# Optimization experiments

Measured on AMD Instinct MI355X. Metric: run time of the kernel, lower is better.

Reference implementation:

```python
import jax, jax.numpy as jnp
import numpy as np

HQ, HKV, D, RD = 32, 8, 128, 64   # q heads, kv heads, head_dim, rotary_dim
EPS = 1e-6


def _rms_norm(x, w, eps):
    # per-head RMSNorm over last dim (non-gemma: scale by w)
    var = jnp.mean(x * x, axis=-1, keepdims=True)
    return x * jax.lax.rsqrt(var + eps) * w


def _partial_rope(x, c, s, rd):
    # x: [T, H, D]; c/s: [T, rd//2]; NeoX half-split rotation on first rd dims
    x1 = x[..., : rd // 2]
    x2 = x[..., rd // 2 : rd]
    c = c[:, None, :]
    s = s[:, None, :]
    return jnp.concatenate([x1 * c - x2 * s, x2 * c + x1 * s, x[..., rd:]], axis=-1)


def setup_inputs() -> dict:
    key = jax.random.key(0)
    ks = jax.random.split(key, 6)
    B, QL, HID, CACHE = 4, 512, 4096, 512
    T = B * QL
    MAXPOS = 4096
    NPAGES, PS, MP = 256, 16, 64  # total pages, page_size, max pages per seq

    hidden_states = jax.random.normal(ks[0], (T, HID), jnp.float32)
    inv = 1.0 / (10000.0 ** (np.arange(0, RD, 2, dtype=np.float64) / RD))
    ang = np.arange(MAXPOS)[:, None] * inv[None, :]
    cos = jnp.asarray(np.cos(ang), jnp.float32)   # [MAXPOS, RD//2]
    sin = jnp.asarray(np.sin(ang), jnp.float32)
    positions = jnp.tile(CACHE + jnp.arange(QL, dtype=jnp.int32), B)  # [T]
    k_cache = jax.random.normal(ks[1], (NPAGES, PS, HKV, D), jnp.float32)
    v_cache = jax.random.normal(ks[2], (NPAGES, PS, HKV, D), jnp.float32)
    page_table = jnp.arange(B * MP, dtype=jnp.int32).reshape(B, MP)
    cache_seqlens = jnp.full((B,), CACHE, jnp.int32)
    cu_seqlens_q = jnp.arange(B + 1, dtype=jnp.int32) * QL
    qkv_weight = jax.random.normal(ks[3], ((HQ + 2 * HKV) * D, HID), jnp.float32) * 0.02
    o_proj_weight = jax.random.normal(ks[4], (HID, HQ * D), jnp.float32) * 0.02
    q_norm_weight = jnp.ones((D,), jnp.float32)
    k_norm_weight = jnp.ones((D,), jnp.float32)
    return dict(hidden_states=hidden_states, cos=cos, sin=sin, positions=positions,
                k_cache=k_cache, v_cache=v_cache, page_table=page_table,
                cache_seqlens=cache_seqlens, cu_seqlens_q=cu_seqlens_q,
                qkv_weight=qkv_weight, o_proj_weight=o_proj_weight,
                q_norm_weight=q_norm_weight, k_norm_weight=k_norm_weight)


def reference(hidden_states, cos, sin, positions, k_cache, v_cache, page_table,
              cache_seqlens, cu_seqlens_q, qkv_weight, o_proj_weight,
              q_norm_weight, k_norm_weight):
    T = hidden_states.shape[0]
    B = cache_seqlens.shape[0]
    QL = T // B                       # equal-length sequences (extend mode)
    PS = k_cache.shape[1]

    # QKV projection + split
    qkv = hidden_states @ qkv_weight.T
    q, k, v = jnp.split(qkv, [HQ * D, (HQ + HKV) * D], axis=-1)

    # per-head QK RMSNorm (q_norm_weight.shape[0] == head_dim branch)
    q = _rms_norm(q.reshape(T, HQ, D), q_norm_weight, EPS)
    k = _rms_norm(k.reshape(T, HKV, D), k_norm_weight, EPS)
    v = v.reshape(T, HKV, D)

    # partial RoPE
    pc, psn = cos[positions], sin[positions]
    q = _partial_rope(q, pc, psn, RD)
    k = _partial_rope(k, pc, psn, RD)

    # paged KV-cache write: absolute slot = cache_seqlens[b] + j
    pos_abs = cache_seqlens[:, None] + jnp.arange(QL, dtype=jnp.int32)[None, :]  # [B,QL]
    pages = jnp.take_along_axis(page_table, pos_abs // PS, axis=1)
    slots = pos_abs % PS
    k_cache = k_cache.at[pages, slots].set(k.reshape(B, QL, HKV, D))
    v_cache = v_cache.at[pages, slots].set(v.reshape(B, QL, HKV, D))

    # gather per-sequence KV from pages: [B, KV, HKV, D]
    KV = page_table.shape[1] * PS
    keys = k_cache[page_table].reshape(B, KV, HKV, D)
    vals = v_cache[page_table].reshape(B, KV, HKV, D)

    # GQA paged attention with causal mask on absolute positions
    G = HQ // HKV
    qh = q.reshape(B, QL, HKV, G, D)
    scale = 1.0 / np.sqrt(D).astype(np.float32)
    scores = jnp.einsum('bqhgd,bkhd->bhgqk', qh, keys) * scale
    kpos = jnp.arange(KV, dtype=jnp.int32)
    mask = kpos[None, None, :] <= pos_abs[:, :, None]                  # [B,QL,KV]
    scores = jnp.where(mask[:, None, None, :, :], scores, -1e30)
    probs = jax.nn.softmax(scores, axis=-1)
    attn = jnp.einsum('bhgqk,bkhd->bqhgd', probs, vals).reshape(T, HQ * D)

    return attn @ o_proj_weight.T
```

## Files before the change

### kernel.cpp

```cpp
#include <hip/hip_runtime.h>

typedef unsigned int   u32;
typedef unsigned short u16;

typedef float  f32x4  __attribute__((ext_vector_type(4)));
typedef u32    u32x4  __attribute__((ext_vector_type(4)));
typedef u16    u16x4  __attribute__((ext_vector_type(4)));
typedef __bf16 bf16x8 __attribute__((ext_vector_type(8)));

union FragU { u16 us[8]; u32x4 q; bf16x8 v; };

__device__ __forceinline__ u32 f2u(float x){ union{float f;u32 u;}c; c.f=x; return c.u; }
__device__ __forceinline__ float u2f(u32 u){ union{float f;u32 u;}c; c.u=u; return c.f; }
__device__ __forceinline__ u16 bfhi(float x){ u32 u=f2u(x); return (u16)((u + 0x7fffu + ((u>>16)&1u))>>16); }
__device__ __forceinline__ float bff(u16 h){ return u2f(((u32)h)<<16); }

__device__ __forceinline__ void gload16(const void* g, void* l){
  __builtin_amdgcn_global_load_lds(
      (const __attribute__((address_space(1))) unsigned int*)g,
      (__attribute__((address_space(3))) unsigned int*)l, 16, 0, 0);
}

__global__ __launch_bounds__(256)
void bf16_pack3(const float* __restrict__ s0, u16* __restrict__ d0, int n0,
                const float* __restrict__ s1, u16* __restrict__ d1, int n1,
                const float* __restrict__ s2, u16* __restrict__ d2, int n2)
{
  const int total = n0 + n1 + n2;
  for (int i = blockIdx.x*256 + threadIdx.x; i < total; i += gridDim.x*256){
    const float* s; u16* d; int j = i;
    if (j < n0)            { s = s0; d = d0; }
    else if (j < n0 + n1)  { s = s1; d = d1; j -= n0; }
    else                   { s = s2; d = d2; j -= n0 + n1; }
    float4 v = reinterpret_cast<const float4*>(s)[j];
    reinterpret_cast<u16x4*>(d)[j] =
      (u16x4){ bfhi(v.x), bfhi(v.y), bfhi(v.z), bfhi(v.w) };
  }
}

__global__ __launch_bounds__(256, 2)
void gemm_pkA2(const u16* __restrict__ A, const u16* __restrict__ B,
               float* __restrict__ C, int M, int N, int K)
{
  extern __shared__ char smem[];
  const int tid  = threadIdx.x;
  const int lane = tid & 63;
  const int w    = tid >> 6;
  const int wm = w >> 1, wn = w & 1;
  const int ln = lane & 15, lg = lane >> 4;

  const int nbm = M >> 7;
  const int nbn = N / 192;
  const int nwg = nbm * nbn;
  const int swz = (blockIdx.x & 7) * (nwg >> 3) + (blockIdx.x >> 3);
  const int bm = swz % nbm, bn = swz / nbm;

  const size_t rb = (size_t)K * 2;
  const int lrow  = lane >> 3;
  const int lslot = (lane & 7) ^ (lrow & 7);
  const char* As0 = (const char*)A + (size_t)(bm*128 + w*8 + lrow)*rb + lslot*16;
  const char* Bs0 = (const char*)B + (size_t)(bn*192 + w*8 + lrow)*rb + lslot*16;

  auto stA = [&](int buf, int t) {
    const char* s = As0 + ((size_t)t << 7);
    char* d = smem + buf*40960 + w*1024;
    gload16(s,           d);
    gload16(s +  32*rb,  d + 4096);
    gload16(s +  64*rb,  d + 8192);
    gload16(s +  96*rb,  d + 12288);
  };
  auto stB = [&](int buf, int t) {
    const char* s = Bs0 + ((size_t)t << 7);
    char* d = smem + buf*40960 + 16384 + w*1024;
    gload16(s,           d);
    gload16(s +  32*rb,  d + 4096);
    gload16(s +  64*rb,  d + 8192);
    gload16(s +  96*rb,  d + 12288);
    gload16(s + 128*rb,  d + 16384);
    gload16(s + 160*rb,  d + 20480);
  };

  f32x4 z = {0.f,0.f,0.f,0.f};
  f32x4 acc[4][6];
  #pragma unroll
  for (int i=0;i<4;i++){
    #pragma unroll
    for (int j=0;j<6;j++) acc[i][j] = z;
  }

  const int nt = K >> 6;
  stA(0, 0); stB(0, 0);
  if (nt > 1) { stB(1, 1);
    asm volatile("s_waitcnt vmcnt(6)" ::: "memory");
  } else {
    asm volatile("s_waitcnt vmcnt(0)" ::: "memory");
  }
  __builtin_amdgcn_s_barrier();
  asm volatile("" ::: "memory");

  const int lx7 = ln & 7;

  for (int t = 0; t < nt; ++t){
    const int cur = t & 1;
    const char* bufc = smem + cur*40960;

    FragU bfr[6][2];
    #pragma unroll
    for (int ni=0; ni<6; ni++){
      const int rofs = 16384 + (wn*96 + ni*16 + ln)*128;
      #pragma unroll
      for (int ks=0; ks<2; ks++)
        bfr[ni][ks].q = *reinterpret_cast<const u32x4*>(bufc + rofs + (((ks*4+lg)^lx7)<<4));
    }
    FragU af[2][2];
    #pragma unroll
    for (int mf=0; mf<2; mf++){
      const int rofs = (wm*64 + mf*16 + ln)*128;
      #pragma unroll
      for (int ks=0; ks<2; ks++)
        af[mf][ks].q = *reinterpret_cast<const u32x4*>(bufc + rofs + (((ks*4+lg)^lx7)<<4));
    }
    if (t+1 < nt) stA(cur^1, t+1);
    __builtin_amdgcn_s_barrier();
    __builtin_amdgcn_s_setprio(1);
    #pragma unroll
    for (int ks=0; ks<2; ks++){
      #pragma unroll
      for (int mf=0; mf<2; mf++){
        #pragma unroll
        for (int ni=0; ni<6; ni++)
          acc[mf][ni] = __builtin_amdgcn_mfma_f32_16x16x32_bf16(af[mf][ks].v, bfr[ni][ks].v, acc[mf][ni], 0,0,0);
      }
    }
    __builtin_amdgcn_s_setprio(0);
    asm volatile("s_waitcnt lgkmcnt(0)" ::: "memory");
    __builtin_amdgcn_s_barrier();

    FragU ag[2][2];
    #pragma unroll
    for (int mf=0; mf<2; mf++){
      const int rofs = (wm*64 + (mf+2)*16 + ln)*128;
      #pragma unroll
      for (int ks=0; ks<2; ks++)
        ag[mf][ks].q = *reinterpret_cast<const u32x4*>(bufc + rofs + (((ks*4+lg)^lx7)<<4));
    }
    if (t+2 < nt) stB(cur, t+2);
    __builtin_amdgcn_s_barrier();
    __builtin_amdgcn_s_setprio(1);
    #pragma unroll
    for (int ks=0; ks<2; ks++){
      #pragma unroll
      for (int mf=0; mf<2; mf++){
        #pragma unroll
        for (int ni=0; ni<6; ni++)
          acc[mf+2][ni] = __builtin_amdgcn_mfma_f32_16x16x32_bf16(ag[mf][ks].v, bfr[ni][ks].v, acc[mf+2][ni], 0,0,0);
      }
    }
    __builtin_amdgcn_s_setprio(0);
    if (t+1 < nt){
      if (t+2 < nt) asm volatile("s_waitcnt vmcnt(6)" ::: "memory");
      else          asm volatile("s_waitcnt vmcnt(0)" ::: "memory");
    }
    __builtin_amdgcn_s_barrier();
    asm volatile("" ::: "memory");
  }

  #pragma unroll
  for (int mi=0; mi<4; mi++){
    #pragma unroll
    for (int ni=0; ni<6; ni++){
      const int row0 = bm*128 + wm*64 + mi*16 + lg*4;
      const int col  = bn*192 + wn*96 + ni*16 + ln;
      #pragma unroll
      for (int r=0; r<4; r++)
        C[(size_t)(row0+r)*N + col] = acc[mi][ni][r];
    }
  }
}

__global__ __launch_bounds__(256, 2)
void gemm_pkB2(const u16* __restrict__ A, const u16* __restrict__ B,
               float* __restrict__ C, int M, int N, int K)
{
  extern __shared__ char smem[];
  const int tid  = threadIdx.x;
  const int lane = tid & 63;
  const int w    = tid >> 6;
  const int wm = w >> 1, wn = w & 1;
  const int ln = lane & 15, lg = lane >> 4;

  const int nbm = M >> 7, nbn = N >> 7;
  const int nwg = nbm * nbn;
  const int swz = (blockIdx.x & 7) * (nwg >> 3) + (blockIdx.x >> 3);
  const int bm = swz % nbm, bn = swz / nbm;

  const size_t rb = (size_t)K * 2;
  const int lrow  = lane >> 3;
  const int lslot = (lane & 7) ^ (lrow & 7);
  const char* As0 = (const char*)A + (size_t)(bm*128 + w*8 + lrow)*rb + lslot*16;
  const char* Bs0 = (const char*)B + (size_t)(bn*128 + w*8 + lrow)*rb + lslot*16;

  auto stA = [&](int buf, int t) {
    const char* s = As0 + ((size_t)t << 7);
    char* d = smem + buf*32768 + w*1024;
    gload16(s,           d);
    gload16(s +  32*rb,  d + 4096);
    gload16(s +  64*rb,  d + 8192);
    gload16(s +  96*rb,  d + 12288);
  };
  auto stB = [&](int buf, int t) {
    const char* s = Bs0 + ((size_t)t << 7);
    char* d = smem + buf*32768 + 16384 + w*1024;
    gload16(s,           d);
    gload16(s +  32*rb,  d + 4096);
    gload16(s +  64*rb,  d + 8192);
    gload16(s +  96*rb,  d + 12288);
  };

  f32x4 z = {0.f,0.f,0.f,0.f};
  f32x4 acc[4][4];
  #pragma unroll
  for (int i=0;i<4;i++){
    #pragma unroll
    for (int j=0;j<4;j++) acc[i][j] = z;
  }

  const int nt = K >> 6;
  stA(0, 0); stB(0, 0);
  if (nt > 1) { stB(1, 1);
    asm volatile("s_waitcnt vmcnt(4)" ::: "memory");
  } else {
    asm volatile("s_waitcnt vmcnt(0)" ::: "memory");
  }
  __builtin_amdgcn_s_barrier();
  asm volatile("" ::: "memory");

  const int lx7 = ln & 7;

  for (int t = 0; t < nt; ++t){
    const int cur = t & 1;
    const char* bufc = smem + cur*32768;

    FragU bfr[4][2];
    #pragma unroll
    for (int ni=0; ni<4; ni++){
      const int rofs = 16384 + (wn*64 + ni*16 + ln)*128;
      #pragma unroll
      for (int ks=0; ks<2; ks++)
        bfr[ni][ks].q = *reinterpret_cast<const u32x4*>(bufc + rofs + (((ks*4+lg)^lx7)<<4));
    }
    FragU af[2][2];
    #pragma unroll
    for (int mf=0; mf<2; mf++){
      const int rofs = (wm*64 + mf*16 + ln)*128;
      #pragma unroll
      for (int ks=0; ks<2; ks++)
        af[mf][ks].q = *reinterpret_cast<const u32x4*>(bufc + rofs + (((ks*4+lg)^lx7)<<4));
    }
    if (t+1 < nt) stA(cur^1, t+1);
    __builtin_amdgcn_s_barrier();
    __builtin_amdgcn_s_setprio(1);
    #pragma unroll
    for (int ks=0; ks<2; ks++){
      #pragma unroll
      for (int mf=0; mf<2; mf++){
        #pragma unroll
        for (int ni=0; ni<4; ni++)
          acc[mf][ni] = __builtin_amdgcn_mfma_f32_16x16x32_bf16(af[mf][ks].v, bfr[ni][ks].v, acc[mf][ni], 0,0,0);
      }
    }
    __builtin_amdgcn_s_setprio(0);
    asm volatile("s_waitcnt lgkmcnt(0)" ::: "memory");
    __builtin_amdgcn_s_barrier();

    FragU ag[2][2];
    #pragma unroll
    for (int mf=0; mf<2; mf++){
      const int rofs = (wm*64 + (mf+2)*16 + ln)*128;
      #pragma unroll
      for (int ks=0; ks<2; ks++)
        ag[mf][ks].q = *reinterpret_cast<const u32x4*>(bufc + rofs + (((ks*4+lg)^lx7)<<4));
    }
    if (t+2 < nt) stB(cur, t+2);
    __builtin_amdgcn_s_barrier();
    __builtin_amdgcn_s_setprio(1);
    #pragma unroll
    for (int ks=0; ks<2; ks++){
      #pragma unroll
      for (int mf=0; mf<2; mf++){
        #pragma unroll
        for (int ni=0; ni<4; ni++)
          acc[mf+2][ni] = __builtin_amdgcn_mfma_f32_16x16x32_bf16(ag[mf][ks].v, bfr[ni][ks].v, acc[mf+2][ni], 0,0,0);
      }
    }
    __builtin_amdgcn_s_setprio(0);
    if (t+1 < nt){
      if (t+2 < nt) asm volatile("s_waitcnt vmcnt(4)" ::: "memory");
      else          asm volatile("s_waitcnt vmcnt(0)" ::: "memory");
    }
    __builtin_amdgcn_s_barrier();
    asm volatile("" ::: "memory");
  }

  #pragma unroll
  for (int mi=0; mi<4; mi++){
    #pragma unroll
    for (int ni=0; ni<4; ni++){
      const int row0 = bm*128 + wm*64 + mi*16 + lg*4;
      const int col  = bn*128 + wn*64 + ni*16 + ln;
      #pragma unroll
      for (int r=0; r<4; r++)
        C[(size_t)(row0+r)*N + col] = acc[mi][ni][r];
    }
  }
}

__global__ __launch_bounds__(256)
void copy_cache(const float* __restrict__ k_cache, const float* __restrict__ v_cache,
                const int* __restrict__ page_table,
                u16* __restrict__ k_all, u16* __restrict__ v_allT)
{
  __shared__ float tb[32][129];
  const int id = blockIdx.x;
  const int jt = id & 31, h = (id>>5)&7, b = id>>8;
  const int tid = threadIdx.x;
  const int j0 = jt*32;
  {
    int r = tid>>3, c = tid&7;
    int j = j0 + r;
    int page = page_table[b*64 + (j>>4)];
    int slot = j & 15;
    const float* ks = k_cache + (size_t)((page*16 + slot)*8 + h)*128;
    const float* vs = v_cache + (size_t)((page*16 + slot)*8 + h)*128;
    u16* kd = k_all + ((size_t)(b*8+h)*1024 + j)*128;
    #pragma unroll
    for (int i=0;i<4;i++){
      int d0 = (c + 8*i)*4;
      float4 k4 = *reinterpret_cast<const float4*>(ks + d0);
      *reinterpret_cast<u16x4*>(kd + d0) =
        (u16x4){ bfhi(k4.x), bfhi(k4.y), bfhi(k4.z), bfhi(k4.w) };
      float4 v4 = *reinterpret_cast<const float4*>(vs + d0);
      tb[r][d0+0]=v4.x; tb[r][d0+1]=v4.y; tb[r][d0+2]=v4.z; tb[r][d0+3]=v4.w;
    }
  }
  __syncthreads();
  {
    int dout = tid>>1, jh = tid&1;
    u16* vd = v_allT + ((size_t)(b*8+h)*128 + dout)*1024 + j0 + jh*16;
    #pragma unroll
    for (int i=0;i<4;i++){
      u16x4 o = { bfhi(tb[jh*16 + i*4 + 0][dout]),
                  bfhi(tb[jh*16 + i*4 + 1][dout]),
                  bfhi(tb[jh*16 + i*4 + 2][dout]),
                  bfhi(tb[jh*16 + i*4 + 3][dout]) };
      *reinterpret_cast<u16x4*>(vd + i*4) = o;
    }
  }
}

__global__ __launch_bounds__(256)
void norm_rope_scatter(float* __restrict__ qkv, const float* __restrict__ cosT,
                       const float* __restrict__ sinT, const int* __restrict__ positions,
                       const int* __restrict__ cache_seqlens,
                       const float* __restrict__ qw, const float* __restrict__ kw,
                       u16* __restrict__ k_all, u16* __restrict__ v_allT)
{
  const int t = blockIdx.x;
  const int lane = threadIdx.x & 63;
  const int w = threadIdx.x >> 6;
  const int b = t >> 9;
  const int q = t & 511;
  const int pos  = positions[t];
  const int cpos = cache_seqlens[b] + q;
  for (int it=0; it<12; ++it){
    int h = it*4 + w;
    float* xp = qkv + (size_t)t*6144 + h*128 + 2*lane;
    float2 x = *reinterpret_cast<const float2*>(xp);
    if (h < 40){
      float ss = x.x*x.x + x.y*x.y;
      #pragma unroll
      for (int mk=1; mk<64; mk<<=1) ss += __shfl_xor(ss, mk);
      float var = ss*(1.0f/128.0f) + 1e-6f;
      float rq = rsqrtf(var);
      rq = rq*(1.5f - 0.5f*var*rq*rq);
      const float* wt = (h<32) ? qw : kw;
      x.x *= rq*wt[2*lane]; x.y *= rq*wt[2*lane+1];
      float px = __shfl_xor(x.x, 16);
      float py = __shfl_xor(x.y, 16);
      if (lane < 32){
        int ci = pos*32 + 2*(lane&15);
        float2 cc = *reinterpret_cast<const float2*>(cosT + ci);
        float2 sc = *reinterpret_cast<const float2*>(sinT + ci);
        if (lane < 16){ x.x = x.x*cc.x - px*sc.x; x.y = x.y*cc.y - py*sc.y; }
        else          { x.x = x.x*cc.x + px*sc.x; x.y = x.y*cc.y + py*sc.y; }
      }
    }
    if (h < 32){
      *reinterpret_cast<float2*>(xp) = x;
    } else if (h < 40){
      u16* kp = k_all + ((size_t)(b*8 + (h-32))*1024 + cpos)*128 + 2*lane;
      kp[0] = bfhi(x.x); kp[1] = bfhi(x.y);
    } else {
      u16* vp = v_allT + ((size_t)(b*8 + (h-40))*128 + 2*lane)*1024 + cpos;
      vp[0]    = bfhi(x.x);
      vp[1024] = bfhi(x.y);
    }
  }
}

__global__ __launch_bounds__(256)
void attn_fused6(const float* __restrict__ qkv, const u16* __restrict__ k_all,
                 const u16* __restrict__ v_allT, const int* __restrict__ cache_seqlens,
                 u16* __restrict__ attnO)
{
  extern __shared__ char smem[];
  const int tid = threadIdx.x, lane = tid&63, w = tid>>6;
  const int ln = lane&15, lg = lane>>4;
  const int id = blockIdx.x;
  const int qt = id & 7, g = (id>>3)&3, kvh = (id>>5)&7, b = id>>8;
  const int cs = cache_seqlens[b];
  const int h  = kvh*4 + g;
  const int q0 = qt*64 + w*16;
  const float SCALE = 0.08838834764831845f;
  f32x4 z = {0.f,0.f,0.f,0.f};

  FragU qf[4];
  {
    const float* qp = qkv + (size_t)(b*512 + q0 + ln)*6144 + h*128;
    #pragma unroll
    for (int ks=0; ks<4; ks++){
      int d0 = ks*32 + lg*8;
      float4 a = *reinterpret_cast<const float4*>(qp + d0);
      float4 c = *reinterpret_cast<const float4*>(qp + d0 + 4);
      qf[ks].q = (u32x4){
        (u32)bfhi(a.x*SCALE) | ((u32)bfhi(a.y*SCALE)<<16),
        (u32)bfhi(a.z*SCALE) | ((u32)bfhi(a.w*SCALE)<<16),
        (u32)bfhi(c.x*SCALE) | ((u32)bfhi(c.y*SCALE)<<16),
        (u32)bfhi(c.z*SCALE) | ((u32)bfhi(c.w*SCALE)<<16) };
    }
  }
  f32x4 O[8];
  #pragma unroll
  for (int i=0;i<8;i++) O[i] = z;
  float lacc[4] = {0.f,0.f,0.f,0.f};
  const int prow0 = cs + q0 + lg*4;
  const int nt = (cs + qt*64 + 64 + 31) >> 5;
  const char* kbase = (const char*)(k_all  + (size_t)(b*8+kvh)*1024*128);
  const char* vbase = (const char*)(v_allT + (size_t)(b*8+kvh)*128*1024);

  auto stK = [&](int buf, int t){
    #pragma unroll
    for (int i=0;i<2;i++){
      int row = i*16 + w*4 + (lane>>4);
      const char* s = kbase + (size_t)(t*32 + row)*256 + (((lane&15) ^ (row&7))<<4);
      gload16(s, smem + buf*8192 + i*4096 + w*1024);
    }
  };
  auto stV = [&](int buf, int t){
    #pragma unroll
    for (int i=0;i<2;i++){
      int row = i*64 + w*16 + (lane>>2);
      int c   = lane & 3;
      const char* s = vbase + (size_t)row*2048 + (size_t)t*64 + ((c ^ ((row>>1)&3))<<4);
      gload16(s, smem + 16384 + buf*8192 + i*4096 + w*1024);
    }
  };

  stK(0, 0); stV(0, 0);
  if (nt > 1){ stK(1, 1); stV(1, 1); }

  for (int tile=0; tile<nt; ++tile){
    const int cur = tile & 1;
    const int kv0 = tile*32;
    if (tile+1 < nt) asm volatile("s_waitcnt vmcnt(4)" ::: "memory");
    else             asm volatile("s_waitcnt vmcnt(0)" ::: "memory");
    __builtin_amdgcn_s_barrier();

    const u16* Kc = (const u16*)(smem + cur*8192);
    f32x4 sa0=z, sa1=z, sb0=z, sb1=z;
    #pragma unroll
    for (int ks=0; ks<2; ks++){
      int so = ((ks*4+lg) ^ (ln&7)) << 3;
      FragU kf0, kf1;
      kf0.q = *reinterpret_cast<const u32x4*>(&Kc[ln*128 + so]);
      kf1.q = *reinterpret_cast<const u32x4*>(&Kc[(16+ln)*128 + so]);
      sa0 = __builtin_amdgcn_mfma_f32_16x16x32_bf16(qf[ks].v, kf0.v, sa0, 0,0,0);
      sa1 = __builtin_amdgcn_mfma_f32_16x16x32_bf16(qf[ks].v, kf1.v, sa1, 0,0,0);
    }
    #pragma unroll
    for (int ks=2; ks<4; ks++){
      int so = ((ks*4+lg) ^ (ln&7)) << 3;
      FragU kf0, kf1;
      kf0.q = *reinterpret_cast<const u32x4*>(&Kc[ln*128 + so]);
      kf1.q = *reinterpret_cast<const u32x4*>(&Kc[(16+ln)*128 + so]);
      sb0 = __builtin_amdgcn_mfma_f32_16x16x32_bf16(qf[ks].v, kf0.v, sb0, 0,0,0);
      sb1 = __builtin_amdgcn_mfma_f32_16x16x32_bf16(qf[ks].v, kf1.v, sb1, 0,0,0);
    }
    f32x4 s[2]; s[0] = sa0 + sb0; s[1] = sa1 + sb1;

    float pv[2][4];
    if (kv0 + 31 <= cs + q0){
      #pragma unroll
      for (int n=0;n<2;n++){
        #pragma unroll
        for (int r=0;r<4;r++) pv[n][r] = __expf(s[n][r]);
      }
    } else {
      #pragma unroll
      for (int n=0;n<2;n++){
        #pragma unroll
        for (int r=0;r<4;r++){
          bool ok = (kv0 + n*16 + ln) <= (prow0 + r);
          pv[n][r] = ok ? __expf(s[n][r]) : 0.f;
        }
      }
    }
    #pragma unroll
    for (int r=0;r<4;r++) lacc[r] += pv[0][r] + pv[1][r];

    #pragma unroll
    for (int n=0;n<2;n++){
      #pragma unroll
      for (int rp=0; rp<2; rp++){
        float p0 = pv[n][rp*2], p1 = pv[n][rp*2+1];
        u32 hpk;
        asm("v_cvt_pk_bf16_f32 %0, %1, %2" : "=v"(hpk) : "v"(p0), "v"(p1));
        int col  = n*16 + ln;
        int row0 = lg*4 + rp*2;
        int b0 = w*1024 + row0*64 + ((((col>>3) ^ ((row0>>1)&3)))<<4) + (col&7)*2;
        *(u16*)(smem + 32768 + b0)      = (u16)hpk;
        *(u16*)(smem + 32768 + b0 + 64) = (u16)(hpk >> 16);
      }
    }
    FragU pa;
    pa.q = *reinterpret_cast<const u32x4*>(
        smem + 32768 + w*1024 + ln*64 + ((lg ^ ((ln>>1)&3))<<4));

    const char* Vb = smem + 16384 + cur*8192;
    #pragma unroll
    for (int nf=0; nf<8; nf++){
      int dr = nf*16 + ln;
      FragU vf;
      vf.q = *reinterpret_cast<const u32x4*>(Vb + dr*64 + ((lg ^ ((dr>>1)&3))<<4));
      O[nf] = __builtin_amdgcn_mfma_f32_16x16x32_bf16(pa.v, vf.v, O[nf], 0,0,0);
    }
    asm volatile("s_waitcnt lgkmcnt(0)" ::: "memory");
    __builtin_amdgcn_s_barrier();
    if (tile+2 < nt){ stK(cur, tile+2); stV(cur, tile+2); }
  }

  #pragma unroll
  for (int off=1; off<16; off<<=1){
    #pragma unroll
    for (int r=0;r<4;r++) lacc[r] += __shfl_xor(lacc[r], off);
  }
  float il[4];
  #pragma unroll
  for (int r=0;r<4;r++) il[r] = 1.0f / lacc[r];
  u16* op = attnO + (size_t)(b*512 + q0 + lg*4)*4096 + h*128 + ln;
  #pragma unroll
  for (int nf=0; nf<8; nf++){
    #pragma unroll
    for (int r=0;r<4;r++)
      op[(size_t)r*4096 + nf*16] = bfhi(O[nf][r] * il[r]);
  }
}

extern "C" void kernel_launch(void* const* d_in, const int* in_sizes, int n_in,
                              void* d_out, int out_size, void* d_ws, size_t ws_size,
                              hipStream_t stream) {
  const float* hidden    = (const float*)d_in[0];
  const float* cosT      = (const float*)d_in[1];
  const float* sinT      = (const float*)d_in[2];
  const int*   positions = (const int*)  d_in[3];
  const float* k_cache   = (const float*)d_in[4];
  const float* v_cache   = (const float*)d_in[5];
  const int*   page_tab  = (const int*)  d_in[6];
  const int*   cache_sl  = (const int*)  d_in[7];
  const float* qkv_w     = (const float*)d_in[9];
  const float* o_w       = (const float*)d_in[10];
  const float* qnw       = (const float*)d_in[11];
  const float* knw       = (const float*)d_in[12];
  float* out = (float*)d_out;

  float* qkv   = (float*)d_ws;
  u16* k_all   = (u16*)(qkv + 12582912);
  u16* v_allT  = k_all  + 4194304;
  u16* attnPk  = v_allT + 4194304;
  u16* hidPk   = attnPk + 8388608;
  u16* qkvwPk  = hidPk  + 8388608;
  u16* owPk    = qkvwPk + 25165824;
  (void)in_sizes; (void)n_in; (void)out_size; (void)ws_size;

  (void)hipFuncSetAttribute(reinterpret_cast<const void*>(gemm_pkA2),
                            hipFuncAttributeMaxDynamicSharedMemorySize, 81920);
  (void)hipFuncSetAttribute(reinterpret_cast<const void*>(gemm_pkB2),
                            hipFuncAttributeMaxDynamicSharedMemorySize, 65536);
  (void)hipFuncSetAttribute(reinterpret_cast<const void*>(attn_fused6),
                            hipFuncAttributeMaxDynamicSharedMemorySize, 36864);

  hipLaunchKernelGGL(bf16_pack3, dim3(2048), dim3(256), 0, stream,
                     hidden, hidPk, 2097152,
                     qkv_w, qkvwPk, 6291456,
                     o_w, owPk, 4194304);
  hipLaunchKernelGGL(copy_cache, dim3(1024), dim3(256), 0, stream,
                     k_cache, v_cache, page_tab, k_all, v_allT);
  hipLaunchKernelGGL(gemm_pkA2, dim3(512), dim3(256), 81920, stream,
                     hidPk, qkvwPk, qkv, 2048, 6144, 4096);
  hipLaunchKernelGGL(norm_rope_scatter, dim3(2048), dim3(256), 0, stream,
                     qkv, cosT, sinT, positions, cache_sl, qnw, knw, k_all, v_allT);
  hipLaunchKernelGGL(attn_fused6, dim3(1024), dim3(256), 36864, stream,
                     qkv, k_all, v_allT, cache_sl, attnPk);
  hipLaunchKernelGGL(gemm_pkB2, dim3(512), dim3(256), 65536, stream,
                     attnPk, owPk, out, 2048, 4096, 4096);
}
```

Measured before the change: 310.4 us.

## Enlarge attention tiles to 128 queries x 64 keys and merge prep kernels

The attention kernel now runs 512-thread blocks covering 128 query rows and streams 64-key KV tiles, with the LDS layouts and swizzles for K, V and P resized to match. Each K/V tile loaded is reused by twice as many query rows, and half as many loop iterations and barriers are needed. The bf16 packing and paged-cache copy kernels are merged into one launch, removing one kernel launch. In exchange, LDS use rises to 80KB and register pressure rises (four score fragments, two P fragments), which may reduce occupancy. Causal masking now works at a coarser tile granularity, so more partially masked work is computed.

```diff
diff --git a/kernel.cpp b/kernel.cpp
--- a/kernel.cpp
+++ b/kernel.cpp
@@ -22,19 +22,61 @@
 }
 
 __global__ __launch_bounds__(256)
-void bf16_pack3(const float* __restrict__ s0, u16* __restrict__ d0, int n0,
-                const float* __restrict__ s1, u16* __restrict__ d1, int n1,
-                const float* __restrict__ s2, u16* __restrict__ d2, int n2)
+void prep_all(const float* __restrict__ s0, u16* __restrict__ d0, int n0,
+              const float* __restrict__ s1, u16* __restrict__ d1, int n1,
+              const float* __restrict__ s2, u16* __restrict__ d2, int n2,
+              const float* __restrict__ k_cache, const float* __restrict__ v_cache,
+              const int* __restrict__ page_table,
+              u16* __restrict__ k_all, u16* __restrict__ v_allT)
 {
-  const int total = n0 + n1 + n2;
-  for (int i = blockIdx.x*256 + threadIdx.x; i < total; i += gridDim.x*256){
-    const float* s; u16* d; int j = i;
-    if (j < n0)            { s = s0; d = d0; }
-    else if (j < n0 + n1)  { s = s1; d = d1; j -= n0; }
-    else                   { s = s2; d = d2; j -= n0 + n1; }
-    float4 v = reinterpret_cast<const float4*>(s)[j];
-    reinterpret_cast<u16x4*>(d)[j] =
-      (u16x4){ bfhi(v.x), bfhi(v.y), bfhi(v.z), bfhi(v.w) };
+  const int tid = threadIdx.x;
+  if (blockIdx.x < 2048){
+    const int total = n0 + n1 + n2;
+    for (int i = blockIdx.x*256 + tid; i < total; i += 2048*256){
+      const float* s; u16* d; int j = i;
+      if (j < n0)            { s = s0; d = d0; }
+      else if (j < n0 + n1)  { s = s1; d = d1; j -= n0; }
+      else                   { s = s2; d = d2; j -= n0 + n1; }
+      float4 v = reinterpret_cast<const float4*>(s)[j];
+      reinterpret_cast<u16x4*>(d)[j] =
+        (u16x4){ bfhi(v.x), bfhi(v.y), bfhi(v.z), bfhi(v.w) };
+    }
+    return;
+  }
+  __shared__ float tb[32][129];
+  const int id = blockIdx.x - 2048;
+  const int jt = id & 31, h = (id>>5)&7, b = id>>8;
+  const int j0 = jt*32;
+  {
+    int r = tid>>3, c = tid&7;
+    int j = j0 + r;
+    int page = page_table[b*64 + (j>>4)];
+    int slot = j & 15;
+    const float* ks = k_cache + (size_t)((page*16 + slot)*8 + h)*128;
+    const float* vs = v_cache + (size_t)((page*16 + slot)*8 + h)*128;
+    u16* kd = k_all + ((size_t)(b*8+h)*1024 + j)*128;
+    #pragma unroll
+    for (int i=0;i<4;i++){
+      int d0i = (c + 8*i)*4;
+      float4 k4 = *reinterpret_cast<const float4*>(ks + d0i);
+      *reinterpret_cast<u16x4*>(kd + d0i) =
+        (u16x4){ bfhi(k4.x), bfhi(k4.y), bfhi(k4.z), bfhi(k4.w) };
+      float4 v4 = *reinterpret_cast<const float4*>(vs + d0i);
+      tb[r][d0i+0]=v4.x; tb[r][d0i+1]=v4.y; tb[r][d0i+2]=v4.z; tb[r][d0i+3]=v4.w;
+    }
+  }
+  __syncthreads();
+  {
+    int dout = tid>>1, jh = tid&1;
+    u16* vd = v_allT + ((size_t)(b*8+h)*128 + dout)*1024 + j0 + jh*16;
+    #pragma unroll
+    for (int i=0;i<4;i++){
+      u16x4 o = { bfhi(tb[jh*16 + i*4 + 0][dout]),
+                  bfhi(tb[jh*16 + i*4 + 1][dout]),
+                  bfhi(tb[jh*16 + i*4 + 2][dout]),
+                  bfhi(tb[jh*16 + i*4 + 3][dout]) };
+      *reinterpret_cast<u16x4*>(vd + i*4) = o;
+    }
   }
 }
 
@@ -311,49 +353,6 @@
       #pragma unroll
       for (int r=0; r<4; r++)
         C[(size_t)(row0+r)*N + col] = acc[mi][ni][r];
-    }
-  }
-}
-
-__global__ __launch_bounds__(256)
-void copy_cache(const float* __restrict__ k_cache, const float* __restrict__ v_cache,
-                const int* __restrict__ page_table,
-                u16* __restrict__ k_all, u16* __restrict__ v_allT)
-{
-  __shared__ float tb[32][129];
-  const int id = blockIdx.x;
-  const int jt = id & 31, h = (id>>5)&7, b = id>>8;
-  const int tid = threadIdx.x;
-  const int j0 = jt*32;
-  {
-    int r = tid>>3, c = tid&7;
-    int j = j0 + r;
-    int page = page_table[b*64 + (j>>4)];
-    int slot = j & 15;
-    const float* ks = k_cache + (size_t)((page*16 + slot)*8 + h)*128;
-    const float* vs = v_cache + (size_t)((page*16 + slot)*8 + h)*128;
-    u16* kd = k_all + ((size_t)(b*8+h)*1024 + j)*128;
-    #pragma unroll
-    for (int i=0;i<4;i++){
-      int d0 = (c + 8*i)*4;
-      float4 k4 = *reinterpret_cast<const float4*>(ks + d0);
-      *reinterpret_cast<u16x4*>(kd + d0) =
-        (u16x4){ bfhi(k4.x), bfhi(k4.y), bfhi(k4.z), bfhi(k4.w) };
-      float4 v4 = *reinterpret_cast<const float4*>(vs + d0);
-      tb[r][d0+0]=v4.x; tb[r][d0+1]=v4.y; tb[r][d0+2]=v4.z; tb[r][d0+3]=v4.w;
-    }
-  }
-  __syncthreads();
-  {
-    int dout = tid>>1, jh = tid&1;
-    u16* vd = v_allT + ((size_t)(b*8+h)*128 + dout)*1024 + j0 + jh*16;
-    #pragma unroll
-    for (int i=0;i<4;i++){
-      u16x4 o = { bfhi(tb[jh*16 + i*4 + 0][dout]),
-                  bfhi(tb[jh*16 + i*4 + 1][dout]),
-                  bfhi(tb[jh*16 + i*4 + 2][dout]),
-                  bfhi(tb[jh*16 + i*4 + 3][dout]) };
-      *reinterpret_cast<u16x4*>(vd + i*4) = o;
     }
   }
 }
@@ -408,8 +407,8 @@
   }
 }
 
-__global__ __launch_bounds__(256)
-void attn_fused6(const float* __restrict__ qkv, const u16* __restrict__ k_all,
+__global__ __launch_bounds__(512)
+void attn_fused8(const float* __restrict__ qkv, const u16* __restrict__ k_all,
                  const u16* __restrict__ v_allT, const int* __restrict__ cache_seqlens,
                  u16* __restrict__ attnO)
 {
@@ -417,10 +416,10 @@
   const int tid = threadIdx.x, lane = tid&63, w = tid>>6;
   const int ln = lane&15, lg = lane>>4;
   const int id = blockIdx.x;
-  const int qt = id & 7, g = (id>>3)&3, kvh = (id>>5)&7, b = id>>8;
+  const int qt = id & 3, g = (id>>2)&3, kvh = (id>>4)&7, b = id>>7;
   const int cs = cache_seqlens[b];
   const int h  = kvh*4 + g;
-  const int q0 = qt*64 + w*16;
+  const int q0 = qt*128 + w*16;
   const float SCALE = 0.08838834764831845f;
   f32x4 z = {0.f,0.f,0.f,0.f};
 
@@ -444,25 +443,24 @@
   for (int i=0;i<8;i++) O[i] = z;
   float lacc[4] = {0.f,0.f,0.f,0.f};
   const int prow0 = cs + q0 + lg*4;
-  const int nt = (cs + qt*64 + 64 + 31) >> 5;
+  const int nt = (cs + qt*128 + 128 + 63) >> 6;
   const char* kbase = (const char*)(k_all  + (size_t)(b*8+kvh)*1024*128);
   const char* vbase = (const char*)(v_allT + (size_t)(b*8+kvh)*128*1024);
 
   auto stK = [&](int buf, int t){
     #pragma unroll
     for (int i=0;i<2;i++){
-      int row = i*16 + w*4 + (lane>>4);
-      const char* s = kbase + (size_t)(t*32 + row)*256 + (((lane&15) ^ (row&7))<<4);
-      gload16(s, smem + buf*8192 + i*4096 + w*1024);
+      int row = i*32 + w*4 + (lane>>4);
+      const char* s = kbase + (size_t)(t*64 + row)*256 + (((lane&15) ^ (row&7))<<4);
+      gload16(s, smem + buf*16384 + i*8192 + w*1024);
     }
   };
   auto stV = [&](int buf, int t){
     #pragma unroll
     for (int i=0;i<2;i++){
-      int row = i*64 + w*16 + (lane>>2);
-      int c   = lane & 3;
-      const char* s = vbase + (size_t)row*2048 + (size_t)t*64 + ((c ^ ((row>>1)&3))<<4);
-      gload16(s, smem + 16384 + buf*8192 + i*4096 + w*1024);
+      int row = i*64 + w*8 + (lane>>3);
+      const char* s = vbase + (size_t)row*2048 + (size_t)t*128 + (((lane&7) ^ (row&7))<<4);
+      gload16(s, smem + 32768 + buf*16384 + i*8192 + w*1024);
     }
   };
 
@@ -471,43 +469,34 @@
 
   for (int tile=0; tile<nt; ++tile){
     const int cur = tile & 1;
-    const int kv0 = tile*32;
+    const int kv0 = tile*64;
     if (tile+1 < nt) asm volatile("s_waitcnt vmcnt(4)" ::: "memory");
     else             asm volatile("s_waitcnt vmcnt(0)" ::: "memory");
     __builtin_amdgcn_s_barrier();
 
-    const u16* Kc = (const u16*)(smem + cur*8192);
-    f32x4 sa0=z, sa1=z, sb0=z, sb1=z;
-    #pragma unroll
-    for (int ks=0; ks<2; ks++){
+    const u16* Kc = (const u16*)(smem + cur*16384);
+    f32x4 s[4]; s[0]=z; s[1]=z; s[2]=z; s[3]=z;
+    #pragma unroll
+    for (int ks=0; ks<4; ks++){
       int so = ((ks*4+lg) ^ (ln&7)) << 3;
-      FragU kf0, kf1;
-      kf0.q = *reinterpret_cast<const u32x4*>(&Kc[ln*128 + so]);
-      kf1.q = *reinterpret_cast<const u32x4*>(&Kc[(16+ln)*128 + so]);
-      sa0 = __builtin_amdgcn_mfma_f32_16x16x32_bf16(qf[ks].v, kf0.v, sa0, 0,0,0);
-      sa1 = __builtin_amdgcn_mfma_f32_16x16x32_bf16(qf[ks].v, kf1.v, sa1, 0,0,0);
-    }
-    #pragma unroll
-    for (int ks=2; ks<4; ks++){
-      int so = ((ks*4+lg) ^ (ln&7)) << 3;
-      FragU kf0, kf1;
-      kf0.q = *reinterpret_cast<const u32x4*>(&Kc[ln*128 + so]);
-      kf1.q = *reinterpret_cast<const u32x4*>(&Kc[(16+ln)*128 + so]);
-      sb0 = __builtin_amdgcn_mfma_f32_16x16x32_bf16(qf[ks].v, kf0.v, sb0, 0,0,0);
-      sb1 = __builtin_amdgcn_mfma_f32_16x16x32_bf16(qf[ks].v, kf1.v, sb1, 0,0,0);
-    }
-    f32x4 s[2]; s[0] = sa0 + sb0; s[1] = sa1 + sb1;
-
-    float pv[2][4];
-    if (kv0 + 31 <= cs + q0){
-      #pragma unroll
-      for (int n=0;n<2;n++){
+      #pragma unroll
+      for (int n=0; n<4; n++){
+        FragU kf;
+        kf.q = *reinterpret_cast<const u32x4*>(&Kc[(n*16+ln)*128 + so]);
+        s[n] = __builtin_amdgcn_mfma_f32_16x16x32_bf16(qf[ks].v, kf.v, s[n], 0,0,0);
+      }
+    }
+
+    float pv[4][4];
+    if (kv0 + 63 <= cs + q0){
+      #pragma unroll
+      for (int n=0;n<4;n++){
         #pragma unroll
         for (int r=0;r<4;r++) pv[n][r] = __expf(s[n][r]);
       }
     } else {
       #pragma unroll
-      for (int n=0;n<2;n++){
+      for (int n=0;n<4;n++){
         #pragma unroll
         for (int r=0;r<4;r++){
           bool ok = (kv0 + n*16 + ln) <= (prow0 + r);
@@ -516,10 +505,10 @@
       }
     }
     #pragma unroll
-    for (int r=0;r<4;r++) lacc[r] += pv[0][r] + pv[1][r];
-
-    #pragma unroll
-    for (int n=0;n<2;n++){
+    for (int r=0;r<4;r++) lacc[r] += (pv[0][r] + pv[1][r]) + (pv[2][r] + pv[3][r]);
+
+    #pragma unroll
+    for (int n=0;n<4;n++){
       #pragma unroll
       for (int rp=0; rp<2; rp++){
         float p0 = pv[n][rp*2], p1 = pv[n][rp*2+1];
@@ -527,22 +516,27 @@
         asm("v_cvt_pk_bf16_f32 %0, %1, %2" : "=v"(hpk) : "v"(p0), "v"(p1));
         int col  = n*16 + ln;
         int row0 = lg*4 + rp*2;
-        int b0 = w*1024 + row0*64 + ((((col>>3) ^ ((row0>>1)&3)))<<4) + (col&7)*2;
-        *(u16*)(smem + 32768 + b0)      = (u16)hpk;
-        *(u16*)(smem + 32768 + b0 + 64) = (u16)(hpk >> 16);
-      }
-    }
-    FragU pa;
-    pa.q = *reinterpret_cast<const u32x4*>(
-        smem + 32768 + w*1024 + ln*64 + ((lg ^ ((ln>>1)&3))<<4));
-
-    const char* Vb = smem + 16384 + cur*8192;
+        int b0 = w*2048 + row0*128 + ((((col>>3) ^ ((row0>>1)&7)))<<4) + (col&7)*2;
+        *(u16*)(smem + 65536 + b0)       = (u16)hpk;
+        *(u16*)(smem + 65536 + b0 + 128) = (u16)(hpk >> 16);
+      }
+    }
+    FragU pa[2];
+    #pragma unroll
+    for (int ks2=0; ks2<2; ks2++)
+      pa[ks2].q = *reinterpret_cast<const u32x4*>(
+          smem + 65536 + w*2048 + ln*128 + (((ks2*4+lg) ^ ((ln>>1)&7))<<4));
+
+    const char* Vb = smem + 32768 + cur*16384;
     #pragma unroll
     for (int nf=0; nf<8; nf++){
       int dr = nf*16 + ln;
-      FragU vf;
-      vf.q = *reinterpret_cast<const u32x4*>(Vb + dr*64 + ((lg ^ ((dr>>1)&3))<<4));
-      O[nf] = __builtin_amdgcn_mfma_f32_16x16x32_bf16(pa.v, vf.v, O[nf], 0,0,0);
+      #pragma unroll
+      for (int ks2=0; ks2<2; ks2++){
+        FragU vf;
+        vf.q = *reinterpret_cast<const u32x4*>(Vb + dr*128 + (((ks2*4+lg) ^ (dr&7))<<4));
+        O[nf] = __builtin_amdgcn_mfma_f32_16x16x32_bf16(pa[ks2].v, vf.v, O[nf], 0,0,0);
+      }
     }
     asm volatile("s_waitcnt lgkmcnt(0)" ::: "memory");
     __builtin_amdgcn_s_barrier();
@@ -596,20 +590,19 @@
                             hipFuncAttributeMaxDynamicSharedMemorySize, 81920);
   (void)hipFuncSetAttribute(reinterpret_cast<const void*>(gemm_pkB2),
                             hipFuncAttributeMaxDynamicSharedMemorySize, 65536);
-  (void)hipFuncSetAttribute(reinterpret_cast<const void*>(attn_fused6),
-                            hipFuncAttributeMaxDynamicSharedMemorySize, 36864);
-
-  hipLaunchKernelGGL(bf16_pack3, dim3(2048), dim3(256), 0, stream,
+  (void)hipFuncSetAttribute(reinterpret_cast<const void*>(attn_fused8),
+                            hipFuncAttributeMaxDynamicSharedMemorySize, 81920);
+
+  hipLaunchKernelGGL(prep_all, dim3(3072), dim3(256), 0, stream,
                      hidden, hidPk, 2097152,
                      qkv_w, qkvwPk, 6291456,
-                     o_w, owPk, 4194304);
-  hipLaunchKernelGGL(copy_cache, dim3(1024), dim3(256), 0, stream,
+                     o_w, owPk, 4194304,
                      k_cache, v_cache, page_tab, k_all, v_allT);
   hipLaunchKernelGGL(gemm_pkA2, dim3(512), dim3(256), 81920, stream,
                      hidPk, qkvwPk, qkv, 2048, 6144, 4096);
   hipLaunchKernelGGL(norm_rope_scatter, dim3(2048), dim3(256), 0, stream,
                      qkv, cosT, sinT, positions, cache_sl, qnw, knw, k_all, v_allT);
-  hipLaunchKernelGGL(attn_fused6, dim3(1024), dim3(256), 36864, stream,
+  hipLaunchKernelGGL(attn_fused8, dim3(512), dim3(512), 81920, stream,
                      qkv, k_all, v_allT, cache_sl, attnPk);
   hipLaunchKernelGGL(gemm_pkB2, dim3(512), dim3(256), 65536, stream,
                      attnPk, owPk, out, 2048, 4096, 4096);
```

Measured after the change: 301.7 us. 1.03x faster.
